# Performance work log

Hardware: AMD Instinct MI355X
Metric: run time of the kernel (lower is better)

The kernel has to match this reference:

```python
import jax, jax.numpy as jnp
import numpy as np

B, L, D, H = 4, 1024, 768, 12
DH = D // H  # 64


def setup_inputs() -> dict:
    key = jax.random.key(0)
    kx, kk, kq, kv = jax.random.split(key, 4)
    # Original uses torch.rand (uniform [0,1)); scale by 1/D so pre-softmax
    # logits stay in a numerically sane range (same math, better conditioning).
    scale = 1.0 / D
    x = jax.random.normal(kx, (B, L, D), dtype=jnp.float32)
    k = jax.random.uniform(kk, (H, D, D), dtype=jnp.float32) * scale
    q = jax.random.uniform(kq, (H, D, D), dtype=jnp.float32) * scale
    v = jax.random.uniform(kv, (H, DH, D), dtype=jnp.float32) * scale
    return {"x": x, "k": k, "q": q, "v": v}


def reference(x, k, q, v):
    # x: [B, L, D]; torch permutes to [B, D, L] then 'bdl,ncd->bncl';
    # equivalent directly: 'bld,ncd->bncl'.
    K = jnp.einsum('bld,ncd->bncl', x, k)   # [B, H, D, L]
    Q = jnp.einsum('bld,ncd->bncl', x, q)   # [B, H, D, L]
    V = jnp.einsum('bld,ncd->bncl', x, v)   # [B, H, DH, L]
    scores = jnp.einsum('bndl,bndm->bnlm', Q, K)        # [B, H, L, L]
    S = jax.nn.softmax(scores, axis=-1)                  # softmax over dim 3
    R = jnp.einsum('bnkl,bndl->bndk', S, V)              # [B, H, DH, L]
    R = R.reshape(x.shape[0], D, -1)                     # [B, D, L]
    return jnp.transpose(R, (0, 2, 1))                   # [B, L, D]
```

## Files before the change

kernel.cpp:

```cpp
#include <hip/hip_runtime.h>
#include <hip/hip_bf16.h>
#include <stdint.h>
#include <stddef.h>

typedef unsigned short u16;
typedef __attribute__((ext_vector_type(8))) short short8;
typedef __attribute__((ext_vector_type(4))) float f32x4;
typedef __attribute__((ext_vector_type(16))) float f32x16;

#define NB 4
#define NL 1024
#define ND 768
#define NH 12
#define NDH 64

__device__ __forceinline__ u16 f2bf(float f) {
  __hip_bfloat16 h = __float2bfloat16(f);
  return *reinterpret_cast<u16*>(&h);
}
__device__ __forceinline__ float bf2f(u16 u) {
  __hip_bfloat16 h;
  *reinterpret_cast<u16*>(&h) = u;
  return __bfloat162float(h);
}

__device__ __forceinline__ void load16_to_lds(const u16* g, u16* l) {
  __builtin_amdgcn_global_load_lds(
      (__attribute__((address_space(1))) void*)(uintptr_t)g,
      (__attribute__((address_space(3))) void*)(uint32_t)(uintptr_t)l,
      16, 0, 0);
}

__global__ __launch_bounds__(256) void cast2_bf16_kernel(const float* __restrict__ inA,
                                                         u16* __restrict__ outA, int n4A,
                                                         const float* __restrict__ inB,
                                                         u16* __restrict__ outB, int n4B) {
  int i = blockIdx.x * 256 + threadIdx.x;
  int stride = gridDim.x * 256;
  int tot = n4A + n4B;
  for (; i < tot; i += stride) {
    const float4* src;
    ushort4* dst;
    int j;
    if (i < n4A) { src = (const float4*)inA; dst = (ushort4*)outA; j = i; }
    else         { src = (const float4*)inB; dst = (ushort4*)outB; j = i - n4A; }
    float4 f = src[j];
    ushort4 o;
    o.x = f2bf(f.x); o.y = f2bf(f.y); o.z = f2bf(f.z); o.w = f2bf(f.w);
    dst[j] = o;
  }
}

__global__ __launch_bounds__(256) void transpose_cast2_kernel(const float* __restrict__ qI,
                                                              const float* __restrict__ kI,
                                                              u16* __restrict__ qT,
                                                              u16* __restrict__ kTp) {
  __shared__ float tile[32][33];
  int hz = blockIdx.z;
  int h = (hz < NH) ? hz : hz - NH;
  const float* src = ((hz < NH) ? qI : kI) + (size_t)h * ND * ND;
  u16* dst = ((hz < NH) ? qT : kTp) + (size_t)h * ND * ND;
  int c0 = blockIdx.x * 32, r0 = blockIdx.y * 32;
  int tx = threadIdx.x & 31, ty = threadIdx.x >> 5;
#pragma unroll
  for (int i = 0; i < 32; i += 8)
    tile[ty + i][tx] = src[(size_t)(r0 + ty + i) * ND + c0 + tx];
  __syncthreads();
#pragma unroll
  for (int i = 0; i < 32; i += 8)
    dst[(size_t)(c0 + ty + i) * ND + r0 + tx] = f2bf(tile[tx][ty + i]);
}

template <bool BF16_OUT, int IM, int IN, int KDIM, int LDC>
__global__ __launch_bounds__(256, 4) void gemm_bt(
    const u16* __restrict__ A, const u16* __restrict__ Bm, void* __restrict__ Cv,
    long sAb, long sAn, long sAz,
    long sBb, long sBn, long sBz,
    long sCb, long sCn, long sCz,
    int p0) {
  constexpr int BK = 64;
  constexpr int MTILE = IM * 64;
  constexpr int NTILE = IN * 64;
  constexpr int CPR = BK / 8;
  constexpr int ACH = MTILE * CPR / 256;
  constexpr int BCH = NTILE * CPR / 256;
  __shared__ __align__(16) u16 As[MTILE * BK];
  __shared__ __align__(16) u16 Bs[NTILE * BK];

  int id = blockIdx.x + gridDim.x * (blockIdx.y + gridDim.y * blockIdx.z);
  int total = gridDim.x * gridDim.y * gridDim.z;
  int xx, yy, zz;
  if ((total & 7) == 0) {
    int per = total >> 3;
    int wk = (id & 7) * per + (id >> 3);
    xx = wk % gridDim.x;
    int g2 = wk / gridDim.x;
    yy = g2 % gridDim.y;
    zz = g2 / gridDim.y;
  } else {
    xx = blockIdx.x; yy = blockIdx.y; zz = blockIdx.z;
  }

  int g = p0 + zz;
  int b = g / NH, n = g % NH;
  A  += (size_t)b * sAb + (size_t)n * sAn + (size_t)zz * sAz;
  Bm += (size_t)b * sBb + (size_t)n * sBn + (size_t)zz * sBz;
  size_t cOff = (size_t)b * sCb + (size_t)n * sCn + (size_t)zz * sCz;

  int m0 = yy * MTILE, n0 = xx * NTILE;
  int t = threadIdx.x;
  int lane = t & 63, w = t >> 6;
  int m32 = lane & 31, kg = lane >> 5;
  int wm = w >> 1, wn = w & 1;

  const u16* gAb;
  const u16* gBb;
  {
    int r = t / CPR;
    int cc = (t & (CPR - 1)) ^ (r & 7);
    gAb = A + (size_t)(m0 + r) * KDIM + cc * 8;
    gBb = Bm + (size_t)(n0 + r) * KDIM + cc * 8;
  }

  f32x16 acc[IM][IN];
#pragma unroll
  for (int i = 0; i < IM; i++)
#pragma unroll
    for (int j = 0; j < IN; j++)
#pragma unroll
      for (int r = 0; r < 16; r++) acc[i][j][r] = 0.f;

#pragma unroll 1
  for (int k0 = 0; k0 < KDIM; k0 += BK) {
    __syncthreads();
#pragma unroll
    for (int u = 0; u < ACH; u++)
      load16_to_lds(gAb + (size_t)u * 32 * KDIM, &As[(size_t)(u * 256 + w * 64) * 8]);
    gAb += BK;
#pragma unroll
    for (int u = 0; u < BCH; u++)
      load16_to_lds(gBb + (size_t)u * 32 * KDIM, &Bs[(size_t)(u * 256 + w * 64) * 8]);
    gBb += BK;
    __syncthreads();

#pragma unroll
    for (int kc = 0; kc < 2; kc++) {
      short8 af[IM][2], bfr[IN][2];
#pragma unroll
      for (int i = 0; i < IM; i++) {
        int row = wm * (IM * 32) + i * 32 + m32;
#pragma unroll
        for (int h = 0; h < 2; h++) {
          int ck = (kc * 4 + h * 2 + kg) ^ (row & 7);
          af[i][h] = *(const short8*)&As[row * BK + ck * 8];
        }
      }
#pragma unroll
      for (int j = 0; j < IN; j++) {
        int row = wn * (IN * 32) + j * 32 + m32;
#pragma unroll
        for (int h = 0; h < 2; h++) {
          int ck = (kc * 4 + h * 2 + kg) ^ (row & 7);
          bfr[j][h] = *(const short8*)&Bs[row * BK + ck * 8];
        }
      }
#pragma unroll
      for (int i = 0; i < IM; i++)
#pragma unroll
        for (int j = 0; j < IN; j++) {
          acc[i][j] = __builtin_amdgcn_mfma_f32_32x32x16_bf16(af[i][0], bfr[j][0], acc[i][j], 0, 0, 0);
          acc[i][j] = __builtin_amdgcn_mfma_f32_32x32x16_bf16(af[i][1], bfr[j][1], acc[i][j], 0, 0, 0);
        }
    }
  }

#pragma unroll
  for (int i = 0; i < IM; i++) {
#pragma unroll
    for (int j = 0; j < IN; j++) {
      int colg = n0 + wn * (IN * 32) + j * 32 + m32;
#pragma unroll
      for (int r = 0; r < 16; r++) {
        int rowg = m0 + wm * (IM * 32) + i * 32 + (r & 3) + 8 * (r >> 2) + 4 * kg;
        float vv = acc[i][j][r];
        if (BF16_OUT) {
          ((u16*)Cv)[cOff + (size_t)rowg * LDC + colg] = f2bf(vv);
        } else {
          ((float*)Cv)[cOff + (size_t)rowg * LDC + colg] = vv;
        }
      }
    }
  }
}

template <bool BF16_OUT, int KDIM, int LDC>
__global__ __launch_bounds__(512, 2) void gemm256_8p(
    const u16* __restrict__ A, const u16* __restrict__ Bm, void* __restrict__ Cv,
    long sAb, long sAn, long sAz,
    long sBb, long sBn, long sBz,
    long sCb, long sCn, long sCz,
    int p0) {
  constexpr int BK = 64;
  constexpr int NT = KDIM / BK;
  constexpr int NC = NT / 2;
  static_assert(KDIM % 128 == 0 && NC >= 2, "need even #K-tiles and >=2 cycles");
  __shared__ __align__(16) u16 As[2][256 * BK];
  __shared__ __align__(16) u16 Bs[2][256 * BK];

  int id = blockIdx.x + gridDim.x * (blockIdx.y + gridDim.y * blockIdx.z);
  int total = gridDim.x * gridDim.y * gridDim.z;
  int xx, yy, zz;
  if ((total & 7) == 0) {
    int per = total >> 3;
    int wk = (id & 7) * per + (id >> 3);
    xx = wk % gridDim.x;
    int g2 = wk / gridDim.x;
    yy = g2 % gridDim.y;
    zz = g2 / gridDim.y;
  } else {
    xx = blockIdx.x; yy = blockIdx.y; zz = blockIdx.z;
  }

  int g = p0 + zz;
  int b = g / NH, n = g % NH;
  A  += (size_t)b * sAb + (size_t)n * sAn + (size_t)zz * sAz;
  Bm += (size_t)b * sBb + (size_t)n * sBn + (size_t)zz * sBz;
  size_t cOff = (size_t)b * sCb + (size_t)n * sCn + (size_t)zz * sCz;

  int m0 = yy * 256, n0 = xx * 256;
  int t = threadIdx.x;
  int lane = t & 63, w = t >> 6;
  int wm = w >> 2, wn = w & 3;
  int l15 = lane & 15, q4 = lane >> 4;

  int r0 = t >> 3;
  int cc0 = (t & 7) ^ (r0 & 7);
  const u16* gA = A + (size_t)(m0 + r0) * KDIM + cc0 * 8;
  const u16* gB = Bm + (size_t)(n0 + r0) * KDIM + cc0 * 8;
  int wslab = w * 512;

#define STG_A1(d, h, u, kt) load16_to_lds( \
    gA + (size_t)((h) * 128 + (u) * 64) * KDIM + (size_t)(kt) * BK, \
    &As[d][((h) * 128 + (u) * 64) * BK + wslab])
#define STG_B1(d, h, u, kt) load16_to_lds( \
    gB + (size_t)((h) * 128 + (u) * 64) * KDIM + (size_t)(kt) * BK, \
    &Bs[d][((h) * 128 + (u) * 64) * BK + wslab])
#define STG_A2(d, h, kt) do { STG_A1(d, h, 0, kt); STG_A1(d, h, 1, kt); } while (0)
#define STG_B2(d, h, kt) do { STG_B1(d, h, 0, kt); STG_B1(d, h, 1, kt); } while (0)

#define READ_A(d, qm, dst) do { \
  _Pragma("unroll") for (int fm = 0; fm < 4; fm++) { \
    int row = (qm) * 128 + wm * 64 + fm * 16 + l15; \
    _Pragma("unroll") for (int ks = 0; ks < 2; ks++) { \
      int ck = (ks * 4 + q4) ^ (row & 7); \
      dst[fm][ks] = *(const short8*)&As[d][row * BK + ck * 8]; \
    } \
  } \
} while (0)

#define READ_B(d, qn, dst) do { \
  _Pragma("unroll") for (int fn = 0; fn < 2; fn++) { \
    int row = (qn) * 128 + wn * 32 + fn * 16 + l15; \
    _Pragma("unroll") for (int ks = 0; ks < 2; ks++) { \
      int ck = (ks * 4 + q4) ^ (row & 7); \
      dst[fn][ks] = *(const short8*)&Bs[d][row * BK + ck * 8]; \
    } \
  } \
} while (0)

#define MF_Q(qm, qn, AR, BR) do { \
  __builtin_amdgcn_s_setprio(1); \
  _Pragma("unroll") for (int ks = 0; ks < 2; ks++) \
    _Pragma("unroll") for (int fm = 0; fm < 4; fm++) \
      _Pragma("unroll") for (int fn = 0; fn < 2; fn++) \
        acc[qm][qn][fm][fn] = __builtin_amdgcn_mfma_f32_16x16x32_bf16( \
            AR[fm][ks], BR[fn][ks], acc[qm][qn][fm][fn], 0, 0, 0); \
  __builtin_amdgcn_s_setprio(0); \
} while (0)

#define PH_SYNC() do { \
  __builtin_amdgcn_s_barrier(); \
  asm volatile("s_waitcnt lgkmcnt(0)" ::: "memory"); \
  __builtin_amdgcn_sched_barrier(0); \
} while (0)
#define PH_END() do { \
  __builtin_amdgcn_s_barrier(); \
  __builtin_amdgcn_sched_barrier(0); \
} while (0)

  f32x4 acc[2][2][4][2];
#pragma unroll
  for (int qm = 0; qm < 2; qm++)
#pragma unroll
    for (int qn = 0; qn < 2; qn++)
#pragma unroll
      for (int fm = 0; fm < 4; fm++)
#pragma unroll
        for (int fn = 0; fn < 2; fn++)
          acc[qm][qn][fm][fn] = (f32x4){0.f, 0.f, 0.f, 0.f};

  STG_A2(0, 0, 0); STG_A2(0, 1, 0);
  STG_B2(0, 0, 0); STG_B2(0, 1, 0);
  STG_A2(1, 0, 1); STG_B2(1, 0, 1);
  asm volatile("s_waitcnt vmcnt(4)" ::: "memory");
  __builtin_amdgcn_s_barrier();
  __builtin_amdgcn_sched_barrier(0);

#pragma unroll 1
  for (int cyc = 0; cyc < NC; ++cyc) {
    int t0 = cyc * 2;
    bool full = (cyc + 1 < NC);
    short8 af0[4][2], af1[4][2], bq0[2][2], bq1[2][2];

    READ_A(0, 0, af0); READ_B(0, 0, bq0);
    STG_A2(1, 1, t0 + 1);
    PH_SYNC(); MF_Q(0, 0, af0, bq0); PH_END();
    READ_B(0, 1, bq1);
    STG_B2(1, 1, t0 + 1);
    PH_SYNC(); MF_Q(0, 1, af0, bq1); PH_END();
    READ_A(0, 1, af1);
    if (full) STG_A2(0, 0, t0 + 2);
    PH_SYNC(); MF_Q(1, 0, af1, bq0); PH_END();
    if (full) STG_B2(0, 0, t0 + 2);
    __builtin_amdgcn_s_barrier();
    MF_Q(1, 1, af1, bq1);
    __builtin_amdgcn_sched_barrier(0);
    if (full) asm volatile("s_waitcnt vmcnt(4)" ::: "memory");
    else      asm volatile("s_waitcnt vmcnt(0)" ::: "memory");
    PH_END();

    READ_A(1, 0, af0); READ_B(1, 0, bq0);
    if (full) STG_A2(0, 1, t0 + 2);
    PH_SYNC(); MF_Q(0, 0, af0, bq0); PH_END();
    READ_B(1, 1, bq1);
    if (full) STG_B2(0, 1, t0 + 2);
    PH_SYNC(); MF_Q(0, 1, af0, bq1); PH_END();
    READ_A(1, 1, af1);
    if (full) STG_A2(1, 0, t0 + 3);
    PH_SYNC(); MF_Q(1, 0, af1, bq0); PH_END();
    if (full) {
      STG_B2(1, 0, t0 + 3);
      __builtin_amdgcn_s_barrier();
      MF_Q(1, 1, af1, bq1);
      __builtin_amdgcn_sched_barrier(0);
      asm volatile("s_waitcnt vmcnt(4)" ::: "memory");
      PH_END();
    } else {
      __builtin_amdgcn_s_barrier();
      MF_Q(1, 1, af1, bq1);
    }
  }

#pragma unroll
  for (int qm = 0; qm < 2; qm++)
#pragma unroll
    for (int qn = 0; qn < 2; qn++)
#pragma unroll
      for (int fm = 0; fm < 4; fm++)
#pragma unroll
        for (int fn = 0; fn < 2; fn++) {
          int colg = n0 + qn * 128 + wn * 32 + fn * 16 + l15;
#pragma unroll
          for (int r = 0; r < 4; r++) {
            int rowg = m0 + qm * 128 + wm * 64 + fm * 16 + q4 * 4 + r;
            float vv = acc[qm][qn][fm][fn][r];
            if (BF16_OUT) {
              ((u16*)Cv)[cOff + (size_t)rowg * LDC + colg] = f2bf(vv);
            } else {
              ((float*)Cv)[cOff + (size_t)rowg * LDC + colg] = vv;
            }
          }
        }
#undef STG_A1
#undef STG_B1
#undef STG_A2
#undef STG_B2
#undef READ_A
#undef READ_B
#undef MF_Q
#undef PH_SYNC
#undef PH_END
}

__global__ __launch_bounds__(256) void softmax_pv_kernel(
    const u16* __restrict__ Sb, const u16* __restrict__ V2, float* __restrict__ out,
    int p0) {
  __shared__ __align__(16) u16 Ps[64 * 128];
  __shared__ __align__(16) u16 Vs[64 * 128];

  int id = blockIdx.x + gridDim.x * blockIdx.y;
  int total = gridDim.x * gridDim.y;
  int xx, zz;
  if ((total & 7) == 0) {
    int per = total >> 3;
    int wk = (id & 7) * per + (id >> 3);
    xx = wk & 15; zz = wk >> 4;
  } else {
    xx = blockIdx.x; zz = blockIdx.y;
  }

  int g = p0 + zz;
  int b = g / NH, n = g % NH;
  const u16* S = Sb + (size_t)zz * NL * NL;
  const u16* V = V2 + (size_t)g * NDH * NL;

  int l0 = xx * 64;
  int t = threadIdx.x;
  int lane = t & 63, w = t >> 6;
  int row16 = lane & 15, q = lane >> 4;
  int rs = row16 & 7;

  f32x4 acc[5];
#pragma unroll
  for (int j = 0; j < 5; j++) acc[j] = (f32x4){0.f, 0.f, 0.f, 0.f};

  short8 onesf;
  {
    short val = (row16 == 0) ? (short)0x3F80 : (short)0;
#pragma unroll
    for (int e = 0; e < 8; e++) onesf[e] = val;
  }

  const u16* ssrc[4];
  const u16* vsrc[4];
#pragma unroll
  for (int u = 0; u < 4; u++) {
    int c = u * 256 + t;
    int r = c >> 4, cc = (c & 15) ^ (r & 7);
    ssrc[u] = S + (size_t)(l0 + r) * NL + cc * 8;
    vsrc[u] = V + (size_t)r * NL + cc * 8;
  }

#pragma unroll 1
  for (int mt = 0; mt < 8; mt++) {
    int mo = mt * 128;
    __syncthreads();
#pragma unroll
    for (int u = 0; u < 4; u++)
      load16_to_lds(ssrc[u] + mo, &Ps[(size_t)(u * 256 + w * 64) * 8]);
#pragma unroll
    for (int u = 0; u < 4; u++)
      load16_to_lds(vsrc[u] + mo, &Vs[(size_t)(u * 256 + w * 64) * 8]);
    __syncthreads();

#pragma unroll
    for (int kk = 0; kk < 4; kk++) {
      int ch = ((kk * 4 + q) ^ rs) * 16;
      int lrow = w * 16 + row16;
      short8 raw = *(const short8*)((const char*)Ps + lrow * 256 + ch);
      short8 af;
#pragma unroll
      for (int e = 0; e < 8; e++) af[e] = (short)f2bf(__expf(bf2f((u16)raw[e])));
      short8 bfr[4];
#pragma unroll
      for (int j = 0; j < 4; j++) {
        int dh = j * 16 + row16;
        bfr[j] = *(const short8*)((const char*)Vs + dh * 256 + ch);
      }
#pragma unroll
      for (int j = 0; j < 4; j++)
        acc[j] = __builtin_amdgcn_mfma_f32_16x16x32_bf16(af, bfr[j], acc[j], 0, 0, 0);
      acc[4] = __builtin_amdgcn_mfma_f32_16x16x32_bf16(af, onesf, acc[4], 0, 0, 0);
    }
  }

#pragma unroll
  for (int r = 0; r < 4; r++) {
    float sum = __shfl(acc[4][r], lane & 48, 64);
    float inv = 1.0f / sum;
    int row = l0 + w * 16 + q * 4 + r;
    float* op = out + ((size_t)b * NL + row) * ND + n * NDH;
#pragma unroll
    for (int j = 0; j < 4; j++)
      op[j * 16 + row16] = acc[j][r] * inv;
  }
}

extern "C" void kernel_launch(void* const* d_in, const int* in_sizes, int n_in,
                              void* d_out, int out_size, void* d_ws, size_t ws_size,
                              hipStream_t stream) {
  (void)in_sizes; (void)n_in; (void)out_size;
  const float* x  = (const float*)d_in[0];
  const float* kI = (const float*)d_in[1];
  const float* qI = (const float*)d_in[2];
  const float* vI = (const float*)d_in[3];
  float* out = (float*)d_out;

  size_t off = 0;
  char* wsb = (char*)d_ws;
  auto alloc = [&](size_t bytes) -> char* {
    char* p = wsb + off;
    off += (bytes + 255) & ~(size_t)255;
    return p;
  };
  u16* xb = (u16*)alloc((size_t)NB * NL * ND * 2);
  u16* vb = (u16*)alloc((size_t)NH * NDH * ND * 2);
  u16* MT = (u16*)alloc((size_t)NH * ND * ND * 2);
  u16* V2 = (u16*)alloc((size_t)NB * NH * NDH * NL * 2);
  size_t fixedSz = off;

  u16* qT = (u16*)alloc((size_t)NH * ND * ND * 2);
  u16* kT = (u16*)alloc((size_t)NH * ND * ND * 2);
  size_t scratchEndQK = off;

  const size_t Tsz  = (size_t)NL * ND * 2;
  const size_t Ssz  = (size_t)NL * NL * 2;
  const size_t perPair = Tsz + Ssz;

  int chunk = NB * NH;
  {
    size_t avail = ws_size > fixedSz ? ws_size - fixedSz : 0;
    size_t maxChunk = avail / perPair;
    if (maxChunk < 1) maxChunk = 1;
    if (maxChunk < (size_t)chunk) {
      int passes = (int)(((size_t)NB * NH + maxChunk - 1) / maxChunk);
      chunk = (NB * NH + passes - 1) / passes;
    }
  }
  off = fixedSz;
  u16* T  = (u16*)alloc((size_t)chunk * Tsz);
  u16* Sb = (u16*)alloc((size_t)chunk * Ssz);
  if (off < scratchEndQK) off = scratchEndQK;

  const long DD  = (long)ND * ND;
  const long LD  = (long)NL * ND;
  const long LL  = (long)NL * NL;
  const long DHL = (long)NDH * NL;

  {
    int n4A = NB * NL * ND / 4;
    int n4B = NH * NDH * ND / 4;
    cast2_bf16_kernel<<<dim3((n4A + n4B + 255) / 256), dim3(256), 0, stream>>>(
        x, xb, n4A, vI, vb, n4B);
  }
  transpose_cast2_kernel<<<dim3(24, 24, 2 * NH), dim3(256), 0, stream>>>(qI, kI, qT, kT);

  gemm_bt<true, 2, 2, 768, ND><<<dim3(6, 6, NH), dim3(256), 0, stream>>>(
      kT, qT, MT,
      0, DD, 0,  0, DD, 0,  0, DD, 0, 0);

  gemm_bt<true, 2, 2, 768, NL><<<dim3(8, 6, NB), dim3(256), 0, stream>>>(
      vb, xb, V2,
      0, 0, 0,  0, 0, LD,  0, 0, (long)NH * DHL, 0);

  for (int p0 = 0; p0 < NB * NH; p0 += chunk) {
    int c = NB * NH - p0;
    if (c > chunk) c = chunk;
    gemm256_8p<true, 768, ND><<<dim3(3, 4, c), dim3(512), 0, stream>>>(
        xb, MT, T,
        LD, 0, 0,  0, DD, 0,  0, 0, LD, p0);
    gemm256_8p<true, 768, NL><<<dim3(4, 4, c), dim3(512), 0, stream>>>(
        T, xb, Sb,
        0, 0, LD,  LD, 0, 0,  0, 0, LL, p0);
    softmax_pv_kernel<<<dim3(16, c), dim3(256), 0, stream>>>(Sb, V2, out, p0);
  }
}
```

Measured before the change: 319.5 us.

## Merge prep GEMMs into one launch, vectorize transpose stores, retile T GEMM

Fuses the two preprocessing GEMMs (k^T q product per head and the V projection) into a single gemm_prep launch. Block ids are remapped so the two kinds of work interleave, and surplus blocks for the smaller problem exit early. The transpose-cast kernel now writes pairs of bf16 values as ushort2 instead of scalar stores. The x·M GEMM switches from the 256-tile 8-wave kernel to the 128-tile gemm_bt kernel with more blocks, trading per-block reuse for more parallelism.

```diff
diff --git a/kernel.cpp b/kernel.cpp
--- a/kernel.cpp
+++ b/kernel.cpp
@@ -66,9 +66,14 @@
   for (int i = 0; i < 32; i += 8)
     tile[ty + i][tx] = src[(size_t)(r0 + ty + i) * ND + c0 + tx];
   __syncthreads();
-#pragma unroll
-  for (int i = 0; i < 32; i += 8)
-    dst[(size_t)(c0 + ty + i) * ND + r0 + tx] = f2bf(tile[tx][ty + i]);
+  int p = tx & 15, j = (tx >> 4) * 8 + ty;
+#pragma unroll
+  for (int i = 0; i < 32; i += 16) {
+    ushort2 o;
+    o.x = f2bf(tile[2 * p][j + i]);
+    o.y = f2bf(tile[2 * p + 1][j + i]);
+    *(ushort2*)&dst[(size_t)(c0 + j + i) * ND + r0 + 2 * p] = o;
+  }
 }
 
 template <bool BF16_OUT, int IM, int IN, int KDIM, int LDC>
@@ -188,6 +193,125 @@
         } else {
           ((float*)Cv)[cOff + (size_t)rowg * LDC + colg] = vv;
         }
+      }
+    }
+  }
+}
+
+__global__ __launch_bounds__(256, 4) void gemm_prep(
+    const u16* __restrict__ kT, const u16* __restrict__ qT, u16* __restrict__ MTp,
+    const u16* __restrict__ vb, const u16* __restrict__ xb, u16* __restrict__ V2p) {
+  constexpr int BK = 64;
+  constexpr int KDIM = ND;
+  constexpr int CPR = BK / 8;
+  constexpr long DD = (long)ND * ND;
+  constexpr long LD = (long)NL * ND;
+  __shared__ __align__(16) u16 As[128 * BK];
+  __shared__ __align__(16) u16 Bs[128 * BK];
+
+  int id = blockIdx.x + gridDim.x * (blockIdx.y + gridDim.y * blockIdx.z);
+  int total = gridDim.x * gridDim.y * gridDim.z;
+  int per = total >> 3;
+  int wk = (id & 7) * per + (id >> 3);
+  int xx = wk % gridDim.x;
+  int g2 = wk / gridDim.x;
+  int yy = g2 % gridDim.y;
+  int zz = g2 / gridDim.y;
+
+  const u16* A;
+  const u16* Bm;
+  u16* C;
+  int ldc;
+  if (zz < NH) {
+    if (xx >= 6) return;
+    A = kT + (size_t)zz * DD;
+    Bm = qT + (size_t)zz * DD;
+    C = MTp + (size_t)zz * DD;
+    ldc = ND;
+  } else {
+    int b = zz - NH;
+    A = vb;
+    Bm = xb + (size_t)b * LD;
+    C = V2p + (size_t)b * NH * NDH * NL;
+    ldc = NL;
+  }
+
+  int m0 = yy * 128, n0 = xx * 128;
+  int t = threadIdx.x;
+  int lane = t & 63, w = t >> 6;
+  int m32 = lane & 31, kg = lane >> 5;
+  int wm = w >> 1, wn = w & 1;
+
+  const u16* gAb;
+  const u16* gBb;
+  {
+    int r = t / CPR;
+    int cc = (t & (CPR - 1)) ^ (r & 7);
+    gAb = A + (size_t)(m0 + r) * KDIM + cc * 8;
+    gBb = Bm + (size_t)(n0 + r) * KDIM + cc * 8;
+  }
+
+  f32x16 acc[2][2];
+#pragma unroll
+  for (int i = 0; i < 2; i++)
+#pragma unroll
+    for (int j = 0; j < 2; j++)
+#pragma unroll
+      for (int r = 0; r < 16; r++) acc[i][j][r] = 0.f;
+
+#pragma unroll 1
+  for (int k0 = 0; k0 < KDIM; k0 += BK) {
+    __syncthreads();
+#pragma unroll
+    for (int u = 0; u < 4; u++)
+      load16_to_lds(gAb + (size_t)u * 32 * KDIM, &As[(size_t)(u * 256 + w * 64) * 8]);
+    gAb += BK;
+#pragma unroll
+    for (int u = 0; u < 4; u++)
+      load16_to_lds(gBb + (size_t)u * 32 * KDIM, &Bs[(size_t)(u * 256 + w * 64) * 8]);
+    gBb += BK;
+    __syncthreads();
+
+#pragma unroll
+    for (int kc = 0; kc < 2; kc++) {
+      short8 af[2][2], bfr[2][2];
+#pragma unroll
+      for (int i = 0; i < 2; i++) {
+        int row = wm * 64 + i * 32 + m32;
+#pragma unroll
+        for (int h = 0; h < 2; h++) {
+          int ck = (kc * 4 + h * 2 + kg) ^ (row & 7);
+          af[i][h] = *(const short8*)&As[row * BK + ck * 8];
+        }
+      }
+#pragma unroll
+      for (int j = 0; j < 2; j++) {
+        int row = wn * 64 + j * 32 + m32;
+#pragma unroll
+        for (int h = 0; h < 2; h++) {
+          int ck = (kc * 4 + h * 2 + kg) ^ (row & 7);
+          bfr[j][h] = *(const short8*)&Bs[row * BK + ck * 8];
+        }
+      }
+#pragma unroll
+      for (int i = 0; i < 2; i++)
+#pragma unroll
+        for (int j = 0; j < 2; j++) {
+          acc[i][j] = __builtin_amdgcn_mfma_f32_32x32x16_bf16(af[i][0], bfr[j][0], acc[i][j], 0, 0, 0);
+          acc[i][j] = __builtin_amdgcn_mfma_f32_32x32x16_bf16(af[i][1], bfr[j][1], acc[i][j], 0, 0, 0);
+        }
+    }
+  }
+
+#pragma unroll
+  for (int i = 0; i < 2; i++) {
+#pragma unroll
+    for (int j = 0; j < 2; j++) {
+      int colg = n0 + wn * 64 + j * 32 + m32;
+#pragma unroll
+      for (int r = 0; r < 16; r++) {
+        int rowg = m0 + wm * 64 + i * 32 + (r & 3) + 8 * (r >> 2) + 4 * kg;
+        C[(size_t)rowg * ldc + colg] = f2bf(acc[i][j][r]);
       }
     }
   }
@@ -525,7 +649,6 @@
   const long DD  = (long)ND * ND;
   const long LD  = (long)NL * ND;
   const long LL  = (long)NL * NL;
-  const long DHL = (long)NDH * NL;
 
   {
     int n4A = NB * NL * ND / 4;
@@ -535,18 +658,12 @@
   }
   transpose_cast2_kernel<<<dim3(24, 24, 2 * NH), dim3(256), 0, stream>>>(qI, kI, qT, kT);
 
-  gemm_bt<true, 2, 2, 768, ND><<<dim3(6, 6, NH), dim3(256), 0, stream>>>(
-      kT, qT, MT,
-      0, DD, 0,  0, DD, 0,  0, DD, 0, 0);
-
-  gemm_bt<true, 2, 2, 768, NL><<<dim3(8, 6, NB), dim3(256), 0, stream>>>(
-      vb, xb, V2,
-      0, 0, 0,  0, 0, LD,  0, 0, (long)NH * DHL, 0);
+  gemm_prep<<<dim3(8, 6, 16), dim3(256), 0, stream>>>(kT, qT, MT, vb, xb, V2);
 
   for (int p0 = 0; p0 < NB * NH; p0 += chunk) {
     int c = NB * NH - p0;
     if (c > chunk) c = chunk;
-    gemm256_8p<true, 768, ND><<<dim3(3, 4, c), dim3(512), 0, stream>>>(
+    gemm_bt<true, 2, 2, 768, ND><<<dim3(6, 8, c), dim3(256), 0, stream>>>(
         xb, MT, T,
         LD, 0, 0,  0, DD, 0,  0, 0, LD, p0);
     gemm256_8p<true, 768, NL><<<dim3(4, 4, c), dim3(512), 0, stream>>>(
```

After: 300.7 us. 5.9% less time.
